# Kernel tuning notes

Measured on AMD Instinct MI355X. Metric: run time of the kernel, lower is better.

## Reference

```python
import jax, jax.numpy as jnp
import numpy as np

VX, VY, VZ = 0.2, 0.2, 4.0
PCR = (0.0, -40.0, -3.0, 70.4, 40.0, 1.0)
X_OFF = VX / 2 + PCR[0]
Y_OFF = VY / 2 + PCR[1]
Z_OFF = VZ / 2 + PCR[2]
BN_EPS = 1e-3
N_POINTS = 600000
N_VOXELS = 60000
CANVAS_X, CANVAS_Y = 352, 400  # (70.4-0)/0.2, (40-(-40))/0.2


def setup_inputs() -> dict:
    key = jax.random.key(0)
    ks = jax.random.split(key, 8)
    rng = np.random.default_rng(0)
    # pick N_VOXELS distinct occupied voxels on the BEV canvas
    lin = rng.permutation(CANVAS_X * CANVAS_Y)[:N_VOXELS]
    inv = rng.integers(0, N_VOXELS, size=N_POINTS)
    inv[:N_VOXELS] = np.arange(N_VOXELS)  # guarantee every voxel occupied
    pv = lin[inv]
    coors = np.zeros((N_POINTS, 4), np.int32)  # (batch, z, y, x)
    coors[:, 3] = pv % CANVAS_X
    coors[:, 2] = pv // CANVAS_X
    # point features: xyz inside point cloud range + intensity
    px = jax.random.uniform(ks[0], (N_POINTS,), minval=PCR[0], maxval=PCR[3])
    py = jax.random.uniform(ks[1], (N_POINTS,), minval=PCR[1], maxval=PCR[4])
    pz = jax.random.uniform(ks[2], (N_POINTS,), minval=PCR[2], maxval=PCR[5])
    pi = jax.random.uniform(ks[3], (N_POINTS,))
    features = jnp.stack([px, py, pz, pi], axis=1)
    return {
        'features': features,
        'w0': jax.random.normal(ks[4], (10, 64)) * 0.3,
        'g0': jnp.ones((64,)),
        'b0': jnp.zeros((64,)),
        'w1': jax.random.normal(ks[5], (128, 128)) * 0.08,
        'g1': jnp.ones((128,)),
        'b1': jnp.zeros((128,)),
        'coors': jnp.asarray(coors),
        'unq_inv': jnp.asarray(inv.astype(np.int32)),
        'num_voxels': N_VOXELS,
    }


def _bn_relu(x, g, b):
    # BN1d training-mode forward: biased batch stats, eps=1e-3
    mu = jnp.mean(x, axis=0)
    var = jnp.mean(jnp.square(x - mu), axis=0)
    return jax.nn.relu((x - mu) * jax.lax.rsqrt(var + BN_EPS) * g + b)


def reference(features, w0, g0, b0, w1, g1, b1, coors, unq_inv, num_voxels):
    n = features.shape[0]
    cf = coors.astype(features.dtype)
    # cluster center: scatter-mean of point features per voxel, gathered back
    vsum = jax.ops.segment_sum(features, unq_inv, num_segments=num_voxels)
    cnt = jax.ops.segment_sum(jnp.ones((n, 1), features.dtype), unq_inv,
                              num_segments=num_voxels)
    voxel_mean = vsum / jnp.maximum(cnt, 1.0)
    f_cluster = features[:, :3] - voxel_mean[unq_inv][:, :3]
    # offset to voxel center (coors layout: batch, z, y, x)
    f_center = jnp.stack([
        features[:, 0] - (cf[:, 3] * VX + X_OFF),
        features[:, 1] - (cf[:, 2] * VY + Y_OFF),
        features[:, 2] - (cf[:, 1] * VZ + Z_OFF),
    ], axis=1)
    x = jnp.concatenate([features, f_cluster, f_center], axis=1)  # [N,10]
    # VFE layer 0 + scatter-max pool + gather-concat
    p0 = _bn_relu(x @ w0, g0, b0)                                  # [N,64]
    v0 = jax.ops.segment_max(p0, unq_inv, num_segments=num_voxels)
    x1 = jnp.concatenate([p0, v0[unq_inv]], axis=1)                # [N,128]
    # VFE layer 1 + final scatter-max pool
    p1 = _bn_relu(x1 @ w1, g1, b1)                                 # [N,128]
    voxel_feats = jax.ops.segment_max(p1, unq_inv, num_segments=num_voxels)
    return voxel_feats  # [M,128]
```

## Files before the change

kernel.cpp:

```cpp
#include <hip/hip_runtime.h>
#include <hip/hip_bf16.h>


typedef __attribute__((ext_vector_type(8))) short bf16x8;
typedef __attribute__((ext_vector_type(4))) float f32x4;
typedef __attribute__((ext_vector_type(4))) int i32x4;
typedef unsigned short u16;
typedef unsigned int u32;

#define RSP 72
#define SCB 2048
#define SPW0 6
#define SPW1 6

__device__ __forceinline__ float bf2f(u16 u) { return __uint_as_float(((u32)u) << 16); }
__device__ __forceinline__ u16 f2bfbits(float f) {
  __hip_bfloat16 h = __float2bfloat16(f);
  return __builtin_bit_cast(u16, h);
}
__device__ __forceinline__ float ldf(const void* p, int i, int flag) {
  return flag ? bf2f(((const u16*)p)[i]) : ((const float*)p)[i];
}
__device__ __forceinline__ u32 encf(float f) {
  u32 b = __float_as_uint(f);
  return b ^ ((u32)(((int)b) >> 31) | 0x80000000u);
}
__device__ __forceinline__ float decf(u32 k) {
  u32 b = (k & 0x80000000u) ? (k ^ 0x80000000u) : ~k;
  return __uint_as_float(b);
}
__device__ __forceinline__ u32 bflyu(u32 x) {
  x = max(x, (u32)__shfl_xor((int)x, 16));
  x = max(x, (u32)__shfl_xor((int)x, 32));
  return x;
}
__device__ __forceinline__ float bflyf(float x) {
  x = fmaxf(x, __shfl_xor(x, 16));
  x = fmaxf(x, __shfl_xor(x, 32));
  return x;
}
__device__ __forceinline__ bf16x8 pack8(float4 a, float4 b) {
  bf16x8 r;
  r[0] = (short)f2bfbits(a.x); r[1] = (short)f2bfbits(a.y);
  r[2] = (short)f2bfbits(a.z); r[3] = (short)f2bfbits(a.w);
  r[4] = (short)f2bfbits(b.x); r[5] = (short)f2bfbits(b.y);
  r[6] = (short)f2bfbits(b.z); r[7] = (short)f2bfbits(b.w);
  return r;
}

__global__ void k_probe(const u32* __restrict__ g0bits, int* __restrict__ flag) {
  if (threadIdx.x == 0 && blockIdx.x == 0)
    flag[0] = (g0bits[0] == 0x3F800000u) ? 0 : 1;
}

__global__ __launch_bounds__(256) void k_pre(
    const void* __restrict__ w0p, const void* __restrict__ w1p,
    const void* __restrict__ g1p,
    u16* __restrict__ w0t, u16* __restrict__ w1t, u32* __restrict__ gsign,
    float4* __restrict__ z4a, long nza4,
    float4* __restrict__ keysws, float4* __restrict__ doutp, long nzk4,
    const int* __restrict__ flagp) {
  const int t = threadIdx.x;
  const int flag = flagp[0];
  if (blockIdx.x == 0) {
    for (int i = t; i < 2048; i += 256) {
      int c = i >> 5, k = i & 31;
      w0t[i] = (k < 10) ? f2bfbits(ldf(w0p, k * 64 + c, flag)) : (u16)0;
    }
    for (int i = t; i < 16384; i += 256) {
      int c = i >> 7, k = i & 127;
      w1t[i] = f2bfbits(ldf(w1p, k * 128 + c, flag));
    }
    if (t < 128) gsign[t] = (ldf(g1p, t, flag) < 0.f) ? 0xFFFFFFFFu : 0u;
  } else {
    float4* keys4 = flag ? keysws : doutp;
    const long total = nza4 + nzk4;
    const long nth = (long)(gridDim.x - 1) * 256;
    const float4 z = {0.f, 0.f, 0.f, 0.f};
    for (long i = (long)(blockIdx.x - 1) * 256 + t; i < total; i += nth) {
      if (i < nza4) z4a[i] = z; else keys4[i - nza4] = z;
    }
  }
}

__global__ __launch_bounds__(256) void k_hist(const int* __restrict__ inv,
                                              unsigned* __restrict__ vcnt, int n) {
  const int stride = gridDim.x * blockDim.x;
  for (int p = blockIdx.x * blockDim.x + threadIdx.x; p < n; p += stride)
    atomicAdd(&vcnt[inv[p]], 1u);
}

__global__ __launch_bounds__(256) void k_scanA(const unsigned* __restrict__ vcnt,
                                               unsigned* __restrict__ bsum, int M) {
  __shared__ unsigned sh[4];
  const int t = threadIdx.x;
  long base = (long)blockIdx.x * SCB;
  unsigned s = 0;
  for (int i = t; i < SCB; i += 256) {
    long idx = base + i;
    s += (idx < M) ? vcnt[idx] : 0u;
  }
  #pragma unroll
  for (int off = 1; off < 64; off <<= 1) s += __shfl_xor(s, off);
  if ((t & 63) == 0) sh[t >> 6] = s;
  __syncthreads();
  if (t == 0) bsum[blockIdx.x] = sh[0] + sh[1] + sh[2] + sh[3];
}

__global__ __launch_bounds__(256) void k_scanB(const unsigned* __restrict__ bsum,
                                               unsigned* __restrict__ boff, int nb) {
  __shared__ unsigned sh[256];
  const int t = threadIdx.x;
  unsigned loc[8];
  unsigned s = 0;
  #pragma unroll
  for (int j = 0; j < 8; ++j) {
    int i = t * 8 + j;
    loc[j] = (i < nb) ? bsum[i] : 0u;
    s += loc[j];
  }
  sh[t] = s; __syncthreads();
  for (int off = 1; off < 256; off <<= 1) {
    unsigned add = (t >= off) ? sh[t - off] : 0u;
    __syncthreads();
    sh[t] += add;
    __syncthreads();
  }
  unsigned excl = sh[t] - s;
  #pragma unroll
  for (int j = 0; j < 8; ++j) {
    int i = t * 8 + j;
    if (i < nb) { boff[i] = excl; excl += loc[j]; }
  }
}

__global__ __launch_bounds__(256) void k_scanC(const unsigned* __restrict__ vcnt,
                                               const unsigned* __restrict__ boff,
                                               unsigned* __restrict__ voff, int M) {
  __shared__ unsigned sh[256];
  const int t = threadIdx.x;
  long base = (long)blockIdx.x * SCB;
  unsigned loc[8];
  unsigned s = 0;
  #pragma unroll
  for (int j = 0; j < 8; ++j) {
    long i = base + t * 8 + j;
    loc[j] = (i < M) ? vcnt[i] : 0u;
    s += loc[j];
  }
  sh[t] = s; __syncthreads();
  for (int off = 1; off < 256; off <<= 1) {
    unsigned add = (t >= off) ? sh[t - off] : 0u;
    __syncthreads();
    sh[t] += add;
    __syncthreads();
  }
  unsigned excl = sh[t] - s + boff[blockIdx.x];
  #pragma unroll
  for (int j = 0; j < 8; ++j) {
    long i = base + t * 8 + j;
    if (i < M) { voff[i] = excl; excl += loc[j]; }
  }
}

__global__ __launch_bounds__(256) void k_fill2(
    const void* __restrict__ feat, const int4* __restrict__ coors4,
    const int* __restrict__ inv, const unsigned* __restrict__ voff,
    unsigned* __restrict__ wcur, u32* __restrict__ rec,
    const int* __restrict__ flagp, int n) {
  const int flag = flagp[0];
  const int stride = gridDim.x * blockDim.x;
  for (int p = blockIdx.x * blockDim.x + threadIdx.x; p < n; p += stride) {
    float fx, fy, fz, fi;
    if (flag) {
      ushort4 f = ((const ushort4*)feat)[p];
      fx = bf2f(f.x); fy = bf2f(f.y); fz = bf2f(f.z); fi = bf2f(f.w);
    } else {
      float4 f = ((const float4*)feat)[p];
      fx = f.x; fy = f.y; fz = f.z; fi = f.w;
    }
    int4 c = coors4[p];
    u32 cp = ((u32)(c.y & 0xFFF) << 20) | ((u32)(c.z & 0x3FF) << 10) | (u32)(c.w & 0x3FF);
    int v = inv[p];
    unsigned pos = voff[v] + atomicAdd(&wcur[v], 1u);
    uint4* dst = (uint4*)(rec + (long)pos * 8);
    uint4 q0 = {__float_as_uint(fx), __float_as_uint(fy), __float_as_uint(fz), __float_as_uint(fi)};
    uint4 q1 = {cp, (u32)v, 0u, 0u};
    dst[0] = q0;
    dst[1] = q1;
  }
}

__global__ __launch_bounds__(256) void k_vsum2(
    const u32* __restrict__ rec, const unsigned* __restrict__ voff,
    const unsigned* __restrict__ vcnt, float* __restrict__ vsum, int M) {
  const int v = blockIdx.x * 256 + threadIdx.x;
  if (v >= M) return;
  const unsigned o = voff[v], c = vcnt[v];
  float sx = 0.f, sy = 0.f, sz = 0.f;
  for (unsigned j = 0; j < c; ++j) {
    const float* rp = (const float*)(rec + (long)(o + j) * 8);
    sx += rp[0]; sy += rp[1]; sz += rp[2];
  }
  vsum[3 * v + 0] = sx;
  vsum[3 * v + 1] = sy;
  vsum[3 * v + 2] = sz;
}

__global__ __launch_bounds__(256) void k_fillx2(
    const u32* __restrict__ rec, const float* __restrict__ vsum,
    const unsigned* __restrict__ vcnt,
    u32* __restrict__ xpk, float* __restrict__ stat0acc, int n) {
  float acc[65];
  #pragma unroll
  for (int j = 0; j < 65; ++j) acc[j] = 0.f;
  const int t = threadIdx.x;
  const int stride = gridDim.x * blockDim.x;
  for (int pos = blockIdx.x * blockDim.x + t; pos < n; pos += stride) {
    const u32* rp = rec + (long)pos * 8;
    uint4 q0 = *(const uint4*)rp;
    uint4 q1 = *(const uint4*)(rp + 4);
    float px = __uint_as_float(q0.x), py = __uint_as_float(q0.y);
    float pz = __uint_as_float(q0.z), pi = __uint_as_float(q0.w);
    const u32 cp = q1.x;
    const int v = (int)q1.y;
    unsigned cn = vcnt[v];
    float ic = 1.f / (float)(cn ? cn : 1u);
    float mx = vsum[3 * v + 0] * ic, my = vsum[3 * v + 1] * ic, mz = vsum[3 * v + 2] * ic;
    float x[10];
    x[0] = px; x[1] = py; x[2] = pz; x[3] = pi;
    x[4] = px - mx; x[5] = py - my; x[6] = pz - mz;
    x[7] = px - ((float)(cp & 0x3FFu) * 0.2f + 0.1f);
    x[8] = py - ((float)((cp >> 10) & 0x3FFu) * 0.2f - 39.9f);
    x[9] = pz - ((float)((cp >> 20) & 0xFFFu) * 4.0f - 1.0f);
    int k = 0;
    #pragma unroll
    for (int a = 0; a < 10; ++a) acc[k++] += x[a];
    #pragma unroll
    for (int a = 0; a < 10; ++a) {
      #pragma unroll
      for (int b = a; b < 10; ++b) acc[k++] += x[a] * x[b];
    }
    u32 u[5];
    #pragma unroll
    for (int j = 0; j < 5; ++j)
      u[j] = (u32)f2bfbits(x[2 * j]) | ((u32)f2bfbits(x[2 * j + 1]) << 16);
    uint4* dst = (uint4*)(xpk + (long)pos * 8);
    uint4 o0 = {u[0], u[1], u[2], u[3]};
    uint4 o1 = {u[4], (u32)v, 0u, 0u};
    dst[0] = o0;
    dst[1] = o1;
  }
  __shared__ float red[65];
  if (t < 65) red[t] = 0.f;
  __syncthreads();
  const int lane = t & 63;
  #pragma unroll
  for (int j = 0; j < 65; ++j) {
    float s = acc[j];
    #pragma unroll
    for (int off = 1; off < 64; off <<= 1) s += __shfl_xor(s, off);
    if (lane == 0) atomicAdd(&red[j], s);
  }
  __syncthreads();
  if (t < 65) atomicAdd(&stat0acc[t], red[t]);
}

__global__ void k_bn0fin(const float* __restrict__ stat0acc,
                         const void* __restrict__ w0p,
                         const void* __restrict__ g0p,
                         const void* __restrict__ b0p,
                         float* __restrict__ a0, float* __restrict__ c0,
                         const int* __restrict__ flagp, int n) {
  const int flag = flagp[0];
  __shared__ float tot[65];
  const int t = threadIdx.x;
  if (t < 65) tot[t] = stat0acc[t];
  __syncthreads();
  if (t < 64) {
    const float invN = 1.0f / (float)n;
    float w[10];
    #pragma unroll
    for (int i = 0; i < 10; ++i) w[i] = ldf(w0p, i * 64 + t, flag);
    float mu = 0.f;
    #pragma unroll
    for (int i = 0; i < 10; ++i) mu += tot[i] * w[i];
    mu *= invN;
    float e2 = 0.f;
    int k = 10;
    #pragma unroll
    for (int a = 0; a < 10; ++a) {
      #pragma unroll
      for (int b = a; b < 10; ++b) {
        float term = tot[k++] * invN * w[a] * w[b];
        e2 += (a == b) ? term : 2.0f * term;
      }
    }
    float var = fmaxf(e2 - mu * mu, 0.f);
    float rs = 1.0f / sqrtf(var + 1e-3f);
    float aa = ldf(g0p, t, flag) * rs;
    a0[t] = aa;
    c0[t] = ldf(b0p, t, flag) - mu * aa;
  }
}

__device__ __forceinline__ bf16x8 l0frag(const u32* __restrict__ xpk,
                                         long grow, long n, int kg) {
  i32x4 ai = {0, 0, 0, 0};
  if (grow < n) {
    const u32* rp = xpk + grow * 8;
    if (kg == 0) {
      uint4 q = *(const uint4*)rp;
      ai[0] = (int)q.x; ai[1] = (int)q.y; ai[2] = (int)q.z; ai[3] = (int)q.w;
    } else if (kg == 1) {
      ai[0] = (int)rp[4];
    }
  }
  return __builtin_bit_cast(bf16x8, ai);
}

__global__ __launch_bounds__(256) void k_l0vox(
    const u32* __restrict__ xpk, const u16* __restrict__ w0t,
    const float* __restrict__ a0, const float* __restrict__ c0,
    float* __restrict__ v0, long n, long nseg, int M) {
  __shared__ int vxs[64];
  __shared__ float pval[2][64];
  __shared__ int pvox[2];
  const int t = threadIdx.x, lane = t & 63, w = t >> 6;
  const int cl = lane & 15, kg = lane >> 4;
  const bf16x8 bw = *(const bf16x8*)(w0t + (16 * w + cl) * 32 + 8 * kg);
  const float al = a0[16 * w + cl], be = c0[16 * w + cl];
  const f32x4 fz = {0.f, 0.f, 0.f, 0.f};
  int curv = -2; float cm = 0.f;
  bool first = true; int fvox = -2; float fcm = 0.f;
  int lastid = -2;
  const long segbase = (long)blockIdx.x * SPW0;
  for (int s = 0; s < SPW0; ++s) {
    const long seg = segbase + s;
    if (seg >= nseg) break;
    const long jb = seg * 64;
    if (t < 64) vxs[t] = (jb + t < n) ? (int)xpk[(jb + t) * 8 + 5] : M;
    __syncthreads();
    for (int mt = 0; mt < 4; ++mt) {
      const long grow = jb + 16 * mt + cl;
      bf16x8 av = l0frag(xpk, grow, n, kg);
      f32x4 a = __builtin_amdgcn_mfma_f32_16x16x32_bf16(av, bw, fz, 0, 0, 0);
      float y[4];
      #pragma unroll
      for (int i2 = 0; i2 < 4; ++i2)
        y[i2] = fmaxf(fmaf(a[i2], al, be), 0.f);
      const int rb = 16 * mt;
      const int rid = vxs[rb + cl];
      const int prid = (cl == 0) ? lastid : vxs[rb + cl - 1];
      const u32 starts = (u32)(__ballot(rid != prid) & 0xFFFFull) | 0x10000u;
      int r = 0;
      while (r < 16) {
        const u32 above = starts & (0xFFFFFFFFu << (r + 1));
        const int e = __ffs(above) - 2;
        const int vrun = __shfl(rid, r);
        float pm = 0.f;
        #pragma unroll
        for (int i2 = 0; i2 < 4; ++i2) {
          const int row = 4 * kg + i2;
          pm = (row >= r && row <= e) ? fmaxf(pm, y[i2]) : pm;
        }
        pm = bflyf(pm);
        if (vrun == curv) cm = fmaxf(cm, pm);
        else {
          if (curv >= 0 && curv < M) {
            if (first) { fvox = curv; fcm = cm; first = false; }
            else if (kg == 0) v0[(long)curv * 64 + 16 * w + cl] = cm;
          }
          curv = vrun; cm = pm;
        }
        r = e + 1;
      }
      lastid = vxs[rb + 15];
    }
    __syncthreads();
  }
  if (t == 0) { pvox[0] = fvox; pvox[1] = curv; }
  if (kg == 0) { pval[0][16 * w + cl] = fcm; pval[1][16 * w + cl] = cm; }
  __syncthreads();
  if (t < 64) {
    int vox = -2; float val = 0.f; bool afirst = true;
    for (int e2 = 0; e2 < 2; ++e2) {
      int ev = pvox[e2];
      if (ev < 0 || ev >= M) continue;
      float evv = pval[e2][t];
      if (ev == vox) val = fmaxf(val, evv);
      else {
        if (vox >= 0) {
          if (afirst) { atomicMax((int*)&v0[(long)vox * 64 + t], __float_as_int(val)); afirst = false; }
          else v0[(long)vox * 64 + t] = val;
        }
        vox = ev; val = evv;
      }
    }
    if (vox >= 0) atomicMax((int*)&v0[(long)vox * 64 + t], __float_as_int(val));
  }
}

__global__ __launch_bounds__(256) void k_v0cvt(const float4* __restrict__ v0,
                                               bf16x8* __restrict__ v0b, long n8) {
  const long stride = (long)gridDim.x * blockDim.x;
  for (long i = (long)blockIdx.x * blockDim.x + threadIdx.x; i < n8; i += stride) {
    float4 f0 = v0[2 * i];
    float4 f1 = v0[2 * i + 1];
    v0b[i] = pack8(f0, f1);
  }
}

__global__ __launch_bounds__(256) void k_vfe1vox(
    const u32* __restrict__ xpk, const u16* __restrict__ w0t,
    const float* __restrict__ a0, const float* __restrict__ c0,
    const u16* __restrict__ w1t, const u32* __restrict__ gsign,
    const u16* __restrict__ v0b,
    u32* __restrict__ keysws, u32* __restrict__ doutk,
    float* __restrict__ stat1acc,
    const int* __restrict__ flagp, long n, long nseg, int M) {
  const int flag = flagp[0];
  u32* keys = flag ? keysws : doutk;
  __shared__ u16 stg[64 * RSP];
  __shared__ int vxs[64];
  __shared__ u32 pval[2][128];
  __shared__ int pvox[2];
  const int t = threadIdx.x, lane = t & 63, w = t >> 6;
  const int cl = lane & 15, kg = lane >> 4;
  const int ct0 = 2 * w, ct1 = 2 * w + 1;
  bf16x8 bw[4];
  float al[4], be[4];
  #pragma unroll
  for (int ct = 0; ct < 4; ++ct) {
    bw[ct] = *(const bf16x8*)(w0t + (16 * ct + cl) * 32 + 8 * kg);
    al[ct] = a0[16 * ct + cl];
    be[ct] = c0[16 * ct + cl];
  }
  const u32 gs0 = gsign[16 * ct0 + cl], gs1 = gsign[16 * ct1 + cl];
  const u16* wr0 = w1t + (16 * ct0 + cl) * 128 + 8 * kg;
  const u16* wr1 = w1t + (16 * ct1 + cl) * 128 + 8 * kg;
  float ssum0 = 0.f, ssq0 = 0.f, ssum1 = 0.f, ssq1 = 0.f;
  const f32x4 fz = {0.f, 0.f, 0.f, 0.f};
  int curv = -2; u32 cm0 = 0, cm1 = 0;
  bool first = true; int fvox = -2; u32 fm0 = 0, fm1 = 0;
  int lastid = -2;
  const long segbase = (long)blockIdx.x * SPW1;

  for (int s = 0; s < SPW1; ++s) {
    const long seg = segbase + s;
    if (seg >= nseg) break;
    const long jb = seg * 64;
    if (t < 64) vxs[t] = (jb + t < n) ? (int)xpk[(jb + t) * 8 + 5] : M;
    {
      const long grow = jb + 16 * w + cl;
      bf16x8 av = l0frag(xpk, grow, n, kg);
      #pragma unroll
      for (int ct = 0; ct < 4; ++ct) {
        f32x4 a = __builtin_amdgcn_mfma_f32_16x16x32_bf16(av, bw[ct], fz, 0, 0, 0);
        #pragma unroll
        for (int i2 = 0; i2 < 4; ++i2) {
          const int lr = 16 * w + 4 * kg + i2;
          float y = fmaxf(fmaf(a[i2], al[ct], be[ct]), 0.f);
          if (jb + lr >= n) y = 0.f;
          stg[lr * RSP + 16 * ct + cl] = f2bfbits(y);
        }
      }
    }
    __syncthreads();
    for (int q = 0; q < 4; ++q) {
      const int lr = 16 * q + cl;
      bf16x8 afr0 = *(const bf16x8*)&stg[lr * RSP + 8 * kg];
      bf16x8 afr1 = *(const bf16x8*)&stg[lr * RSP + 32 + 8 * kg];
      const int vv = vxs[lr];
      const u16* vb = v0b + (long)vv * 64;
      bf16x8 afr2 = *(const bf16x8*)(vb + 8 * kg);
      bf16x8 afr3 = *(const bf16x8*)(vb + 32 + 8 * kg);
      f32x4 acc0 = fz, acc1 = fz;
      {
        bf16x8 b0 = *(const bf16x8*)(wr0);
        bf16x8 b1 = *(const bf16x8*)(wr0 + 32);
        bf16x8 b2 = *(const bf16x8*)(wr0 + 64);
        bf16x8 b3 = *(const bf16x8*)(wr0 + 96);
        acc0 = __builtin_amdgcn_mfma_f32_16x16x32_bf16(afr0, b0, acc0, 0, 0, 0);
        acc0 = __builtin_amdgcn_mfma_f32_16x16x32_bf16(afr1, b1, acc0, 0, 0, 0);
        acc0 = __builtin_amdgcn_mfma_f32_16x16x32_bf16(afr2, b2, acc0, 0, 0, 0);
        acc0 = __builtin_amdgcn_mfma_f32_16x16x32_bf16(afr3, b3, acc0, 0, 0, 0);
      }
      {
        bf16x8 b0 = *(const bf16x8*)(wr1);
        bf16x8 b1 = *(const bf16x8*)(wr1 + 32);
        bf16x8 b2 = *(const bf16x8*)(wr1 + 64);
        bf16x8 b3 = *(const bf16x8*)(wr1 + 96);
        acc1 = __builtin_amdgcn_mfma_f32_16x16x32_bf16(afr0, b0, acc1, 0, 0, 0);
        acc1 = __builtin_amdgcn_mfma_f32_16x16x32_bf16(afr1, b1, acc1, 0, 0, 0);
        acc1 = __builtin_amdgcn_mfma_f32_16x16x32_bf16(afr2, b2, acc1, 0, 0, 0);
        acc1 = __builtin_amdgcn_mfma_f32_16x16x32_bf16(afr3, b3, acc1, 0, 0, 0);
      }
      u32 e0[4], e1[4];
      #pragma unroll
      for (int i2 = 0; i2 < 4; ++i2) {
        float ya = acc0[i2], yb = acc1[i2];
        if (jb + 16 * q + 4 * kg + i2 >= n) { ya = 0.f; yb = 0.f; }
        ssum0 += ya; ssq0 += ya * ya;
        ssum1 += yb; ssq1 += yb * yb;
        e0[i2] = encf(ya) ^ gs0;
        e1[i2] = encf(yb) ^ gs1;
      }
      const int rb = 16 * q;
      const int rid = vxs[rb + cl];
      const int prid = (cl == 0) ? lastid : vxs[rb + cl - 1];
      const u32 starts = (u32)(__ballot(rid != prid) & 0xFFFFull) | 0x10000u;
      int r = 0;
      while (r < 16) {
        const u32 above = starts & (0xFFFFFFFFu << (r + 1));
        const int e = __ffs(above) - 2;
        const int vrun = __shfl(rid, r);
        u32 p0m = 0, p1m = 0;
        #pragma unroll
        for (int i2 = 0; i2 < 4; ++i2) {
          const int row = 4 * kg + i2;
          const bool in = (row >= r) && (row <= e);
          p0m = in ? max(p0m, e0[i2]) : p0m;
          p1m = in ? max(p1m, e1[i2]) : p1m;
        }
        p0m = bflyu(p0m);
        p1m = bflyu(p1m);
        if (vrun == curv) { cm0 = max(cm0, p0m); cm1 = max(cm1, p1m); }
        else {
          if (curv >= 0 && curv < M) {
            if (first) { fvox = curv; fm0 = cm0; fm1 = cm1; first = false; }
            else if (kg == 0) {
              u32* row = keys + (long)curv * 128;
              row[16 * ct0 + cl] = cm0;
              row[16 * ct1 + cl] = cm1;
            }
          }
          curv = vrun; cm0 = p0m; cm1 = p1m;
        }
        r = e + 1;
      }
      lastid = vxs[rb + 15];
    }
    __syncthreads();
  }
  if (t == 0) { pvox[0] = fvox; pvox[1] = curv; }
  if (kg == 0) {
    pval[0][16 * ct0 + cl] = fm0; pval[0][16 * ct1 + cl] = fm1;
    pval[1][16 * ct0 + cl] = cm0; pval[1][16 * ct1 + cl] = cm1;
  }
  __syncthreads();
  if (t < 128) {
    int vox = -2; u32 val = 0; bool afirst = true;
    for (int e2 = 0; e2 < 2; ++e2) {
      int ev = pvox[e2];
      if (ev < 0 || ev >= M) continue;
      u32 evv = pval[e2][t];
      if (ev == vox) val = max(val, evv);
      else {
        if (vox >= 0) {
          if (afirst) { atomicMax(&keys[(long)vox * 128 + t], val); afirst = false; }
          else keys[(long)vox * 128 + t] = val;
        }
        vox = ev; val = evv;
      }
    }
    if (vox >= 0) atomicMax(&keys[(long)vox * 128 + t], val);
  }
  ssum0 += __shfl_xor(ssum0, 16); ssum0 += __shfl_xor(ssum0, 32);
  ssq0 += __shfl_xor(ssq0, 16); ssq0 += __shfl_xor(ssq0, 32);
  ssum1 += __shfl_xor(ssum1, 16); ssum1 += __shfl_xor(ssum1, 32);
  ssq1 += __shfl_xor(ssq1, 16); ssq1 += __shfl_xor(ssq1, 32);
  if (kg == 0) {
    atomicAdd(&stat1acc[16 * ct0 + cl], ssum0);
    atomicAdd(&stat1acc[16 * ct1 + cl], ssum1);
    atomicAdd(&stat1acc[128 + 16 * ct0 + cl], ssq0);
    atomicAdd(&stat1acc[128 + 16 * ct1 + cl], ssq1);
  }
}

__global__ void k_bn1fin(const float* __restrict__ stat1acc,
                         const void* __restrict__ g1p,
                         const void* __restrict__ b1p,
                         float* __restrict__ a1, float* __restrict__ c1,
                         const int* __restrict__ flagp, int n) {
  const int flag = flagp[0];
  const int c = threadIdx.x;
  float s = stat1acc[c];
  float q = stat1acc[128 + c];
  const float invN = 1.0f / (float)n;
  float mu = s * invN;
  float var = fmaxf(q * invN - mu * mu, 0.f);
  float rs = 1.0f / sqrtf(var + 1e-3f);
  float aa = ldf(g1p, c, flag) * rs;
  a1[c] = aa;
  c1[c] = ldf(b1p, c, flag) - mu * aa;
}

__global__ __launch_bounds__(256) void k_fin(
    const u32* __restrict__ keysws, u32* __restrict__ doutk,
    const float* __restrict__ a1, const float* __restrict__ c1,
    const u32* __restrict__ gsign, void* __restrict__ dout,
    const int* __restrict__ flagp, int m32) {
  const int flag = flagp[0];
  const uint4* src = (const uint4*)(flag ? keysws : doutk);
  const int stride = gridDim.x * blockDim.x;
  for (int i = blockIdx.x * blockDim.x + threadIdx.x; i < m32; i += stride) {
    uint4 k = src[i];
    const int cb = (i * 4) & 127;
    float z0 = fmaxf(fmaf(decf(k.x ^ gsign[cb + 0]), a1[cb + 0], c1[cb + 0]), 0.f);
    float z1 = fmaxf(fmaf(decf(k.y ^ gsign[cb + 1]), a1[cb + 1], c1[cb + 1]), 0.f);
    float z2 = fmaxf(fmaf(decf(k.z ^ gsign[cb + 2]), a1[cb + 2], c1[cb + 2]), 0.f);
    float z3 = fmaxf(fmaf(decf(k.w ^ gsign[cb + 3]), a1[cb + 3], c1[cb + 3]), 0.f);
    if (flag) {
      ushort4 o;
      o.x = f2bfbits(z0); o.y = f2bfbits(z1); o.z = f2bfbits(z2); o.w = f2bfbits(z3);
      ((ushort4*)dout)[i] = o;
    } else {
      float4 o = {z0, z1, z2, z3};
      ((float4*)dout)[i] = o;
    }
  }
}

extern "C" void kernel_launch(void* const* d_in, const int* in_sizes, int n_in,
                              void* d_out, int out_size, void* d_ws, size_t ws_size,
                              hipStream_t stream) {
  (void)n_in; (void)ws_size;
  const int n = in_sizes[0] / 4;
  const int M = out_size / 128;
  const long nseg = (n + 63) >> 6;
  const int nb = (M + SCB - 1) / SCB;
  const int nblk0 = (int)((nseg + SPW0 - 1) / SPW0);
  const int nblk1 = (int)((nseg + SPW1 - 1) / SPW1);
  const int nbv = (M + 255) / 256;
  if (n <= 0 || M <= 0) return;

  const void* feat = d_in[0];
  const void* w0p = d_in[1];
  const void* g0p = d_in[2];
  const void* b0p = d_in[3];
  const void* w1p = d_in[4];
  const void* g1p = d_in[5];
  const void* b1p = d_in[6];
  const int4* coors4 = (const int4*)d_in[7];
  const int* inv = (const int*)d_in[8];

  char* wsb = (char*)d_ws;
  long off = 0;
  auto alloc = [&](long bytes) -> void* {
    void* p = wsb + off;
    off = (off + bytes + 255) & ~255L;
    return p;
  };
  int* flagp = (int*)alloc(256);
  float* a0 = (float*)alloc(256);
  float* c0 = (float*)alloc(256);
  float* a1 = (float*)alloc(512);
  float* c1 = (float*)alloc(512);
  u32* gsign = (u32*)alloc(512);
  u16* w0t = (u16*)alloc(2048 * 2);
  u16* w1t = (u16*)alloc(16384 * 2);
  unsigned* bsum = (unsigned*)alloc(2048 * 4);
  unsigned* boff = (unsigned*)alloc(2048 * 4);
  unsigned* voff = (unsigned*)alloc((long)M * 4);
  float* vsum = (float*)alloc((long)M * 3 * 4);
  u32* rec = (u32*)alloc((long)nseg * 64 * 32);
  u32* xpk = (u32*)alloc((long)nseg * 64 * 32);
  u16* v0b = (u16*)alloc((long)(M + 1) * 64 * 2);
  const long nza = 384L + M + (long)(M + 1) * 64 + M;
  float* zbase = (float*)alloc(((nza + 3) / 4) * 16);
  float* stat0acc = zbase;
  float* stat1acc = zbase + 80;
  unsigned* vcnt = (unsigned*)(zbase + 384);
  float* v0 = (float*)(vcnt + M);
  unsigned* wcur = (unsigned*)(v0 + (long)(M + 1) * 64);
  u32* keysws = (u32*)alloc((long)M * 128 * 4);

  hipLaunchKernelGGL(k_probe, dim3(1), dim3(64), 0, stream, (const u32*)g0p, flagp);
  hipLaunchKernelGGL(k_pre, dim3(2048), dim3(256), 0, stream,
                     w0p, w1p, g1p, w0t, w1t, gsign,
                     (float4*)zbase, (nza + 3) / 4,
                     (float4*)keysws, (float4*)d_out, (long)M * 32, flagp);
  hipLaunchKernelGGL(k_hist, dim3(1024), dim3(256), 0, stream, inv, vcnt, n);
  hipLaunchKernelGGL(k_scanA, dim3(nb), dim3(256), 0, stream, vcnt, bsum, M);
  hipLaunchKernelGGL(k_scanB, dim3(1), dim3(256), 0, stream, bsum, boff, nb);
  hipLaunchKernelGGL(k_scanC, dim3(nb), dim3(256), 0, stream, vcnt, boff, voff, M);
  hipLaunchKernelGGL(k_fill2, dim3(1024), dim3(256), 0, stream,
                     feat, coors4, inv, voff, wcur, rec, flagp, n);
  hipLaunchKernelGGL(k_vsum2, dim3(nbv), dim3(256), 0, stream,
                     rec, voff, vcnt, vsum, M);
  hipLaunchKernelGGL(k_fillx2, dim3(1024), dim3(256), 0, stream,
                     rec, vsum, vcnt, xpk, stat0acc, n);
  hipLaunchKernelGGL(k_bn0fin, dim3(1), dim3(128), 0, stream,
                     stat0acc, w0p, g0p, b0p, a0, c0, flagp, n);
  hipLaunchKernelGGL(k_l0vox, dim3(nblk0), dim3(256), 0, stream,
                     xpk, w0t, a0, c0, v0, (long)n, nseg, M);
  hipLaunchKernelGGL(k_v0cvt, dim3(512), dim3(256), 0, stream,
                     (const float4*)v0, (bf16x8*)v0b, (long)(M + 1) * 8);
  hipLaunchKernelGGL(k_vfe1vox, dim3(nblk1), dim3(256), 0, stream,
                     xpk, w0t, a0, c0, w1t, gsign, v0b,
                     keysws, (u32*)d_out, stat1acc, flagp, (long)n, nseg, M);
  hipLaunchKernelGGL(k_bn1fin, dim3(1), dim3(128), 0, stream,
                     stat1acc, g1p, b1p, a1, c1, flagp, n);
  hipLaunchKernelGGL(k_fin, dim3(1024), dim3(256), 0, stream,
                     keysws, (u32*)d_out, a1, c1, gsign, d_out, flagp, M * 32);
}
```

Baseline: 383.2 us.

## Give each wavefront its own segments in layer-0 and layer-1 voxel kernels

Restructures k_l0vox and k_vfe1vox so each wavefront handles its own run of 64-point segments and computes all output channels itself. Previously the four waves of a block split channels and shared staging through LDS with block-wide barriers. Segment voxel ids are now read per lane and neighbours found with shuffles, and layer-1 stages its activation through a per-wave LDS tile with the MFMA operands swapped. The goal is to remove __syncthreads and cross-wave LDS traffic, at the cost of more registers per thread and twice as many boundary atomicMax operations per block.

```diff
diff --git a/kernel.cpp b/kernel.cpp
--- a/kernel.cpp
+++ b/kernel.cpp
@@ -8,10 +8,10 @@
 typedef unsigned short u16;
 typedef unsigned int u32;
 
-#define RSP 72
 #define SCB 2048
 #define SPW0 6
 #define SPW1 6
+#define TRS 72
 
 __device__ __forceinline__ float bf2f(u16 u) { return __uint_as_float(((u32)u) << 16); }
 __device__ __forceinline__ u16 f2bfbits(float f) {
@@ -39,13 +39,8 @@
   x = fmaxf(x, __shfl_xor(x, 32));
   return x;
 }
-__device__ __forceinline__ bf16x8 pack8(float4 a, float4 b) {
-  bf16x8 r;
-  r[0] = (short)f2bfbits(a.x); r[1] = (short)f2bfbits(a.y);
-  r[2] = (short)f2bfbits(a.z); r[3] = (short)f2bfbits(a.w);
-  r[4] = (short)f2bfbits(b.x); r[5] = (short)f2bfbits(b.y);
-  r[6] = (short)f2bfbits(b.z); r[7] = (short)f2bfbits(b.w);
-  return r;
+__device__ __forceinline__ u32 packbf(float a, float b) {
+  return (u32)f2bfbits(a) | ((u32)f2bfbits(b) << 16);
 }
 
 __global__ void k_probe(const u32* __restrict__ g0bits, int* __restrict__ flag) {
@@ -244,7 +239,7 @@
     u32 u[5];
     #pragma unroll
     for (int j = 0; j < 5; ++j)
-      u[j] = (u32)f2bfbits(x[2 * j]) | ((u32)f2bfbits(x[2 * j + 1]) << 16);
+      u[j] = packbf(x[2 * j], x[2 * j + 1]);
     uint4* dst = (uint4*)(xpk + (long)pos * 8);
     uint4 o0 = {u[0], u[1], u[2], u[3]};
     uint4 o1 = {u[4], (u32)v, 0u, 0u};
@@ -323,91 +318,109 @@
     const u32* __restrict__ xpk, const u16* __restrict__ w0t,
     const float* __restrict__ a0, const float* __restrict__ c0,
     float* __restrict__ v0, long n, long nseg, int M) {
-  __shared__ int vxs[64];
-  __shared__ float pval[2][64];
-  __shared__ int pvox[2];
   const int t = threadIdx.x, lane = t & 63, w = t >> 6;
   const int cl = lane & 15, kg = lane >> 4;
-  const bf16x8 bw = *(const bf16x8*)(w0t + (16 * w + cl) * 32 + 8 * kg);
-  const float al = a0[16 * w + cl], be = c0[16 * w + cl];
+  bf16x8 bw[4];
+  float al[4], be[4];
+  #pragma unroll
+  for (int ct = 0; ct < 4; ++ct) {
+    bw[ct] = *(const bf16x8*)(w0t + (16 * ct + cl) * 32 + 8 * kg);
+    al[ct] = a0[16 * ct + cl];
+    be[ct] = c0[16 * ct + cl];
+  }
   const f32x4 fz = {0.f, 0.f, 0.f, 0.f};
-  int curv = -2; float cm = 0.f;
-  bool first = true; int fvox = -2; float fcm = 0.f;
+  int curv = -2;
+  float cm[4] = {0.f, 0.f, 0.f, 0.f};
+  bool first = true; int fvox = -2;
+  float fm[4] = {0.f, 0.f, 0.f, 0.f};
   int lastid = -2;
-  const long segbase = (long)blockIdx.x * SPW0;
+  const long seg0 = ((long)blockIdx.x * 4 + w) * SPW0;
   for (int s = 0; s < SPW0; ++s) {
-    const long seg = segbase + s;
+    const long seg = seg0 + s;
     if (seg >= nseg) break;
     const long jb = seg * 64;
-    if (t < 64) vxs[t] = (jb + t < n) ? (int)xpk[(jb + t) * 8 + 5] : M;
-    __syncthreads();
+    #pragma unroll
     for (int mt = 0; mt < 4; ++mt) {
-      const long grow = jb + 16 * mt + cl;
-      bf16x8 av = l0frag(xpk, grow, n, kg);
-      f32x4 a = __builtin_amdgcn_mfma_f32_16x16x32_bf16(av, bw, fz, 0, 0, 0);
-      float y[4];
+      const long prow = jb + 16 * mt + cl;
+      const int rid = (prow < n) ? (int)xpk[prow * 8 + 5] : M;
+      bf16x8 av = l0frag(xpk, prow, n, kg);
+      float y[4][4];
       #pragma unroll
-      for (int i2 = 0; i2 < 4; ++i2)
-        y[i2] = fmaxf(fmaf(a[i2], al, be), 0.f);
-      const int rb = 16 * mt;
-      const int rid = vxs[rb + cl];
-      const int prid = (cl == 0) ? lastid : vxs[rb + cl - 1];
+      for (int ct = 0; ct < 4; ++ct) {
+        f32x4 p = __builtin_amdgcn_mfma_f32_16x16x32_bf16(av, bw[ct], fz, 0, 0, 0);
+        #pragma unroll
+        for (int i2 = 0; i2 < 4; ++i2) {
+          float yy = fmaxf(fmaf(p[i2], al[ct], be[ct]), 0.f);
+          if (jb + 16 * mt + 4 * kg + i2 >= n) yy = 0.f;
+          y[ct][i2] = yy;
+        }
+      }
+      int prid = __shfl(rid, lane - 1);
+      if (cl == 0) prid = lastid;
       const u32 starts = (u32)(__ballot(rid != prid) & 0xFFFFull) | 0x10000u;
       int r = 0;
       while (r < 16) {
         const u32 above = starts & (0xFFFFFFFFu << (r + 1));
         const int e = __ffs(above) - 2;
         const int vrun = __shfl(rid, r);
-        float pm = 0.f;
+        float pm[4];
         #pragma unroll
-        for (int i2 = 0; i2 < 4; ++i2) {
-          const int row = 4 * kg + i2;
-          pm = (row >= r && row <= e) ? fmaxf(pm, y[i2]) : pm;
+        for (int ct = 0; ct < 4; ++ct) {
+          float q = 0.f;
+          #pragma unroll
+          for (int i2 = 0; i2 < 4; ++i2) {
+            const int row = 4 * kg + i2;
+            q = (row >= r && row <= e) ? fmaxf(q, y[ct][i2]) : q;
+          }
+          pm[ct] = bflyf(q);
         }
-        pm = bflyf(pm);
-        if (vrun == curv) cm = fmaxf(cm, pm);
-        else {
+        if (vrun == curv) {
+          #pragma unroll
+          for (int ct = 0; ct < 4; ++ct) cm[ct] = fmaxf(cm[ct], pm[ct]);
+        } else {
           if (curv >= 0 && curv < M) {
-            if (first) { fvox = curv; fcm = cm; first = false; }
-            else if (kg == 0) v0[(long)curv * 64 + 16 * w + cl] = cm;
+            if (first) {
+              fvox = curv;
+              #pragma unroll
+              for (int ct = 0; ct < 4; ++ct) fm[ct] = cm[ct];
+              first = false;
+            } else if (kg == 0) {
+              #pragma unroll
+              for (int ct = 0; ct < 4; ++ct)
+                v0[(long)curv * 64 + 16 * ct + cl] = cm[ct];
+            }
           }
-          curv = vrun; cm = pm;
+          curv = vrun;
+          #pragma unroll
+          for (int ct = 0; ct < 4; ++ct) cm[ct] = pm[ct];
         }
         r = e + 1;
       }
-      lastid = vxs[rb + 15];
-    }
-    __syncthreads();
-  }
-  if (t == 0) { pvox[0] = fvox; pvox[1] = curv; }
-  if (kg == 0) { pval[0][16 * w + cl] = fcm; pval[1][16 * w + cl] = cm; }
-  __syncthreads();
-  if (t < 64) {
-    int vox = -2; float val = 0.f; bool afirst = true;
-    for (int e2 = 0; e2 < 2; ++e2) {
-      int ev = pvox[e2];
-      if (ev < 0 || ev >= M) continue;
-      float evv = pval[e2][t];
-      if (ev == vox) val = fmaxf(val, evv);
-      else {
-        if (vox >= 0) {
-          if (afirst) { atomicMax((int*)&v0[(long)vox * 64 + t], __float_as_int(val)); afirst = false; }
-          else v0[(long)vox * 64 + t] = val;
-        }
-        vox = ev; val = evv;
-      }
-    }
-    if (vox >= 0) atomicMax((int*)&v0[(long)vox * 64 + t], __float_as_int(val));
-  }
-}
-
-__global__ __launch_bounds__(256) void k_v0cvt(const float4* __restrict__ v0,
-                                               bf16x8* __restrict__ v0b, long n8) {
+      lastid = __shfl(rid, 15);
+    }
+  }
+  if (fvox >= 0 && fvox < M && kg == 0) {
+    #pragma unroll
+    for (int ct = 0; ct < 4; ++ct)
+      atomicMax((int*)&v0[(long)fvox * 64 + 16 * ct + cl], __float_as_int(fm[ct]));
+  }
+  if (curv >= 0 && curv < M && kg == 0) {
+    #pragma unroll
+    for (int ct = 0; ct < 4; ++ct)
+      atomicMax((int*)&v0[(long)curv * 64 + 16 * ct + cl], __float_as_int(cm[ct]));
+  }
+}
+
+__global__ __launch_bounds__(256) void k_v0cvt(const float* __restrict__ v0,
+                                               u32* __restrict__ v0b32, long n8) {
   const long stride = (long)gridDim.x * blockDim.x;
   for (long i = (long)blockIdx.x * blockDim.x + threadIdx.x; i < n8; i += stride) {
-    float4 f0 = v0[2 * i];
-    float4 f1 = v0[2 * i + 1];
-    v0b[i] = pack8(f0, f1);
+    float4 f0 = *(const float4*)(v0 + 8 * i);
+    float4 f1 = *(const float4*)(v0 + 8 * i + 4);
+    uint4 o;
+    o.x = packbf(f0.x, f0.y); o.y = packbf(f0.z, f0.w);
+    o.z = packbf(f1.x, f1.y); o.w = packbf(f1.z, f1.w);
+    *(uint4*)(v0b32 + 4 * i) = o;
   }
 }
 
@@ -421,160 +434,209 @@
     const int* __restrict__ flagp, long n, long nseg, int M) {
   const int flag = flagp[0];
   u32* keys = flag ? keysws : doutk;
-  __shared__ u16 stg[64 * RSP];
-  __shared__ int vxs[64];
-  __shared__ u32 pval[2][128];
-  __shared__ int pvox[2];
+  __shared__ __align__(16) u16 tbuf[4][16 * TRS];
   const int t = threadIdx.x, lane = t & 63, w = t >> 6;
   const int cl = lane & 15, kg = lane >> 4;
-  const int ct0 = 2 * w, ct1 = 2 * w + 1;
+  u16* tb = tbuf[w];
   bf16x8 bw[4];
-  float al[4], be[4];
+  f32x4 alq[4], beq[4];
   #pragma unroll
   for (int ct = 0; ct < 4; ++ct) {
     bw[ct] = *(const bf16x8*)(w0t + (16 * ct + cl) * 32 + 8 * kg);
-    al[ct] = a0[16 * ct + cl];
-    be[ct] = c0[16 * ct + cl];
-  }
-  const u32 gs0 = gsign[16 * ct0 + cl], gs1 = gsign[16 * ct1 + cl];
-  const u16* wr0 = w1t + (16 * ct0 + cl) * 128 + 8 * kg;
-  const u16* wr1 = w1t + (16 * ct1 + cl) * 128 + 8 * kg;
-  float ssum0 = 0.f, ssq0 = 0.f, ssum1 = 0.f, ssq1 = 0.f;
+    alq[ct] = *(const f32x4*)(a0 + 16 * ct + 4 * kg);
+    beq[ct] = *(const f32x4*)(c0 + 16 * ct + 4 * kg);
+  }
+  u32 gsv[8];
+  #pragma unroll
+  for (int ct = 0; ct < 8; ++ct) gsv[ct] = gsign[16 * ct + cl];
+  float ssum[8], ssq[8];
+  #pragma unroll
+  for (int j = 0; j < 8; ++j) { ssum[j] = 0.f; ssq[j] = 0.f; }
   const f32x4 fz = {0.f, 0.f, 0.f, 0.f};
-  int curv = -2; u32 cm0 = 0, cm1 = 0;
-  bool first = true; int fvox = -2; u32 fm0 = 0, fm1 = 0;
+
+  int curvA = -2, curvB = -2;
+  u32 cmA[4] = {0, 0, 0, 0}, cmB[4] = {0, 0, 0, 0};
+  bool firstA = true, firstB = true;
+  int fvoxA = -2, fvoxB = -2;
+  u32 fmA[4] = {0, 0, 0, 0}, fmB[4] = {0, 0, 0, 0};
   int lastid = -2;
-  const long segbase = (long)blockIdx.x * SPW1;
+  const long seg0 = ((long)blockIdx.x * 4 + w) * SPW1;
 
   for (int s = 0; s < SPW1; ++s) {
-    const long seg = segbase + s;
+    const long seg = seg0 + s;
     if (seg >= nseg) break;
     const long jb = seg * 64;
-    if (t < 64) vxs[t] = (jb + t < n) ? (int)xpk[(jb + t) * 8 + 5] : M;
-    {
-      const long grow = jb + 16 * w + cl;
-      bf16x8 av = l0frag(xpk, grow, n, kg);
+    #pragma unroll
+    for (int mt = 0; mt < 4; ++mt) {
+      const long prow = jb + 16 * mt + cl;
+      const int rid = (prow < n) ? (int)xpk[prow * 8 + 5] : M;
+      bf16x8 av = l0frag(xpk, prow, n, kg);
       #pragma unroll
       for (int ct = 0; ct < 4; ++ct) {
-        f32x4 a = __builtin_amdgcn_mfma_f32_16x16x32_bf16(av, bw[ct], fz, 0, 0, 0);
+        f32x4 p = __builtin_amdgcn_mfma_f32_16x16x32_bf16(bw[ct], av, fz, 0, 0, 0);
+        float y0 = fmaxf(fmaf(p[0], alq[ct][0], beq[ct][0]), 0.f);
+        float y1 = fmaxf(fmaf(p[1], alq[ct][1], beq[ct][1]), 0.f);
+        float y2 = fmaxf(fmaf(p[2], alq[ct][2], beq[ct][2]), 0.f);
+        float y3 = fmaxf(fmaf(p[3], alq[ct][3], beq[ct][3]), 0.f);
+        if (prow >= n) { y0 = 0.f; y1 = 0.f; y2 = 0.f; y3 = 0.f; }
+        uint2 pr = {packbf(y0, y1), packbf(y2, y3)};
+        *(uint2*)&tb[cl * TRS + 16 * ct + 4 * kg] = pr;
+      }
+      bf16x8 afr0 = *(const bf16x8*)&tb[cl * TRS + 8 * kg];
+      bf16x8 afr1 = *(const bf16x8*)&tb[cl * TRS + 32 + 8 * kg];
+      const u16* vb = v0b + (long)rid * 64;
+      bf16x8 afr2 = *(const bf16x8*)(vb + 8 * kg);
+      bf16x8 afr3 = *(const bf16x8*)(vb + 32 + 8 * kg);
+      bool padr[4];
+      #pragma unroll
+      for (int i2 = 0; i2 < 4; ++i2) padr[i2] = (jb + 16 * mt + 4 * kg + i2 >= n);
+      int prid = __shfl(rid, lane - 1);
+      if (cl == 0) prid = lastid;
+      const u32 starts = (u32)(__ballot(rid != prid) & 0xFFFFull) | 0x10000u;
+      {
+        u32 eh[4][4];
         #pragma unroll
-        for (int i2 = 0; i2 < 4; ++i2) {
-          const int lr = 16 * w + 4 * kg + i2;
-          float y = fmaxf(fmaf(a[i2], al[ct], be[ct]), 0.f);
-          if (jb + lr >= n) y = 0.f;
-          stg[lr * RSP + 16 * ct + cl] = f2bfbits(y);
+        for (int ct = 0; ct < 4; ++ct) {
+          const u16* wr = w1t + (16 * ct + cl) * 128 + 8 * kg;
+          f32x4 a = fz;
+          a = __builtin_amdgcn_mfma_f32_16x16x32_bf16(afr0, *(const bf16x8*)(wr), a, 0, 0, 0);
+          a = __builtin_amdgcn_mfma_f32_16x16x32_bf16(afr1, *(const bf16x8*)(wr + 32), a, 0, 0, 0);
+          a = __builtin_amdgcn_mfma_f32_16x16x32_bf16(afr2, *(const bf16x8*)(wr + 64), a, 0, 0, 0);
+          a = __builtin_amdgcn_mfma_f32_16x16x32_bf16(afr3, *(const bf16x8*)(wr + 96), a, 0, 0, 0);
+          #pragma unroll
+          for (int i2 = 0; i2 < 4; ++i2) {
+            float yy = padr[i2] ? 0.f : a[i2];
+            ssum[ct] += yy; ssq[ct] += yy * yy;
+            eh[ct][i2] = encf(yy) ^ gsv[ct];
+          }
+        }
+        int r = 0;
+        while (r < 16) {
+          const u32 above = starts & (0xFFFFFFFFu << (r + 1));
+          const int e = __ffs(above) - 2;
+          const int vrun = __shfl(rid, r);
+          u32 pm[4];
+          #pragma unroll
+          for (int ct = 0; ct < 4; ++ct) {
+            u32 q = 0;
+            #pragma unroll
+            for (int i2 = 0; i2 < 4; ++i2) {
+              const int row = 4 * kg + i2;
+              q = (row >= r && row <= e) ? max(q, eh[ct][i2]) : q;
+            }
+            pm[ct] = bflyu(q);
+          }
+          if (vrun == curvA) {
+            #pragma unroll
+            for (int ct = 0; ct < 4; ++ct) cmA[ct] = max(cmA[ct], pm[ct]);
+          } else {
+            if (curvA >= 0 && curvA < M) {
+              if (firstA) {
+                fvoxA = curvA;
+                #pragma unroll
+                for (int ct = 0; ct < 4; ++ct) fmA[ct] = cmA[ct];
+                firstA = false;
+              } else if (kg == 0) {
+                u32* row = keys + (long)curvA * 128;
+                #pragma unroll
+                for (int ct = 0; ct < 4; ++ct) row[16 * ct + cl] = cmA[ct];
+              }
+            }
+            curvA = vrun;
+            #pragma unroll
+            for (int ct = 0; ct < 4; ++ct) cmA[ct] = pm[ct];
+          }
+          r = e + 1;
         }
       }
-    }
-    __syncthreads();
-    for (int q = 0; q < 4; ++q) {
-      const int lr = 16 * q + cl;
-      bf16x8 afr0 = *(const bf16x8*)&stg[lr * RSP + 8 * kg];
-      bf16x8 afr1 = *(const bf16x8*)&stg[lr * RSP + 32 + 8 * kg];
-      const int vv = vxs[lr];
-      const u16* vb = v0b + (long)vv * 64;
-      bf16x8 afr2 = *(const bf16x8*)(vb + 8 * kg);
-      bf16x8 afr3 = *(const bf16x8*)(vb + 32 + 8 * kg);
-      f32x4 acc0 = fz, acc1 = fz;
       {
-        bf16x8 b0 = *(const bf16x8*)(wr0);
-        bf16x8 b1 = *(const bf16x8*)(wr0 + 32);
-        bf16x8 b2 = *(const bf16x8*)(wr0 + 64);
-        bf16x8 b3 = *(const bf16x8*)(wr0 + 96);
-        acc0 = __builtin_amdgcn_mfma_f32_16x16x32_bf16(afr0, b0, acc0, 0, 0, 0);
-        acc0 = __builtin_amdgcn_mfma_f32_16x16x32_bf16(afr1, b1, acc0, 0, 0, 0);
-        acc0 = __builtin_amdgcn_mfma_f32_16x16x32_bf16(afr2, b2, acc0, 0, 0, 0);
-        acc0 = __builtin_amdgcn_mfma_f32_16x16x32_bf16(afr3, b3, acc0, 0, 0, 0);
+        u32 eh[4][4];
+        #pragma unroll
+        for (int ct = 0; ct < 4; ++ct) {
+          const u16* wr = w1t + (16 * (ct + 4) + cl) * 128 + 8 * kg;
+          f32x4 a = fz;
+          a = __builtin_amdgcn_mfma_f32_16x16x32_bf16(afr0, *(const bf16x8*)(wr), a, 0, 0, 0);
+          a = __builtin_amdgcn_mfma_f32_16x16x32_bf16(afr1, *(const bf16x8*)(wr + 32), a, 0, 0, 0);
+          a = __builtin_amdgcn_mfma_f32_16x16x32_bf16(afr2, *(const bf16x8*)(wr + 64), a, 0, 0, 0);
+          a = __builtin_amdgcn_mfma_f32_16x16x32_bf16(afr3, *(const bf16x8*)(wr + 96), a, 0, 0, 0);
+          #pragma unroll
+          for (int i2 = 0; i2 < 4; ++i2) {
+            float yy = padr[i2] ? 0.f : a[i2];
+            ssum[ct + 4] += yy; ssq[ct + 4] += yy * yy;
+            eh[ct][i2] = encf(yy) ^ gsv[ct + 4];
+          }
+        }
+        int r = 0;
+        while (r < 16) {
+          const u32 above = starts & (0xFFFFFFFFu << (r + 1));
+          const int e = __ffs(above) - 2;
+          const int vrun = __shfl(rid, r);
+          u32 pm[4];
+          #pragma unroll
+          for (int ct = 0; ct < 4; ++ct) {
+            u32 q = 0;
+            #pragma unroll
+            for (int i2 = 0; i2 < 4; ++i2) {
+              const int row = 4 * kg + i2;
+              q = (row >= r && row <= e) ? max(q, eh[ct][i2]) : q;
+            }
+            pm[ct] = bflyu(q);
+          }
+          if (vrun == curvB) {
+            #pragma unroll
+            for (int ct = 0; ct < 4; ++ct) cmB[ct] = max(cmB[ct], pm[ct]);
+          } else {
+            if (curvB >= 0 && curvB < M) {
+              if (firstB) {
+                fvoxB = curvB;
+                #pragma unroll
+                for (int ct = 0; ct < 4; ++ct) fmB[ct] = cmB[ct];
+                firstB = false;
+              } else if (kg == 0) {
+                u32* row = keys + (long)curvB * 128;
+                #pragma unroll
+                for (int ct = 0; ct < 4; ++ct) row[64 + 16 * ct + cl] = cmB[ct];
+              }
+            }
+            curvB = vrun;
+            #pragma unroll
+            for (int ct = 0; ct < 4; ++ct) cmB[ct] = pm[ct];
+          }
+          r = e + 1;
+        }
       }
-      {
-        bf16x8 b0 = *(const bf16x8*)(wr1);
-        bf16x8 b1 = *(const bf16x8*)(wr1 + 32);
-        bf16x8 b2 = *(const bf16x8*)(wr1 + 64);
-        bf16x8 b3 = *(const bf16x8*)(wr1 + 96);
-        acc1 = __builtin_amdgcn_mfma_f32_16x16x32_bf16(afr0, b0, acc1, 0, 0, 0);
-        acc1 = __builtin_amdgcn_mfma_f32_16x16x32_bf16(afr1, b1, acc1, 0, 0, 0);
-        acc1 = __builtin_amdgcn_mfma_f32_16x16x32_bf16(afr2, b2, acc1, 0, 0, 0);
-        acc1 = __builtin_amdgcn_mfma_f32_16x16x32_bf16(afr3, b3, acc1, 0, 0, 0);
-      }
-      u32 e0[4], e1[4];
-      #pragma unroll
-      for (int i2 = 0; i2 < 4; ++i2) {
-        float ya = acc0[i2], yb = acc1[i2];
-        if (jb + 16 * q + 4 * kg + i2 >= n) { ya = 0.f; yb = 0.f; }
-        ssum0 += ya; ssq0 += ya * ya;
-        ssum1 += yb; ssq1 += yb * yb;
-        e0[i2] = encf(ya) ^ gs0;
-        e1[i2] = encf(yb) ^ gs1;
-      }
-      const int rb = 16 * q;
-      const int rid = vxs[rb + cl];
-      const int prid = (cl == 0) ? lastid : vxs[rb + cl - 1];
-      const u32 starts = (u32)(__ballot(rid != prid) & 0xFFFFull) | 0x10000u;
-      int r = 0;
-      while (r < 16) {
-        const u32 above = starts & (0xFFFFFFFFu << (r + 1));
-        const int e = __ffs(above) - 2;
-        const int vrun = __shfl(rid, r);
-        u32 p0m = 0, p1m = 0;
-        #pragma unroll
-        for (int i2 = 0; i2 < 4; ++i2) {
-          const int row = 4 * kg + i2;
-          const bool in = (row >= r) && (row <= e);
-          p0m = in ? max(p0m, e0[i2]) : p0m;
-          p1m = in ? max(p1m, e1[i2]) : p1m;
-        }
-        p0m = bflyu(p0m);
-        p1m = bflyu(p1m);
-        if (vrun == curv) { cm0 = max(cm0, p0m); cm1 = max(cm1, p1m); }
-        else {
-          if (curv >= 0 && curv < M) {
-            if (first) { fvox = curv; fm0 = cm0; fm1 = cm1; first = false; }
-            else if (kg == 0) {
-              u32* row = keys + (long)curv * 128;
-              row[16 * ct0 + cl] = cm0;
-              row[16 * ct1 + cl] = cm1;
-            }
-          }
-          curv = vrun; cm0 = p0m; cm1 = p1m;
-        }
-        r = e + 1;
-      }
-      lastid = vxs[rb + 15];
-    }
-    __syncthreads();
-  }
-  if (t == 0) { pvox[0] = fvox; pvox[1] = curv; }
-  if (kg == 0) {
-    pval[0][16 * ct0 + cl] = fm0; pval[0][16 * ct1 + cl] = fm1;
-    pval[1][16 * ct0 + cl] = cm0; pval[1][16 * ct1 + cl] = cm1;
-  }
-  __syncthreads();
-  if (t < 128) {
-    int vox = -2; u32 val = 0; bool afirst = true;
-    for (int e2 = 0; e2 < 2; ++e2) {
-      int ev = pvox[e2];
-      if (ev < 0 || ev >= M) continue;
-      u32 evv = pval[e2][t];
-      if (ev == vox) val = max(val, evv);
-      else {
-        if (vox >= 0) {
-          if (afirst) { atomicMax(&keys[(long)vox * 128 + t], val); afirst = false; }
-          else keys[(long)vox * 128 + t] = val;
-        }
-        vox = ev; val = evv;
-      }
-    }
-    if (vox >= 0) atomicMax(&keys[(long)vox * 128 + t], val);
-  }
-  ssum0 += __shfl_xor(ssum0, 16); ssum0 += __shfl_xor(ssum0, 32);
-  ssq0 += __shfl_xor(ssq0, 16); ssq0 += __shfl_xor(ssq0, 32);
-  ssum1 += __shfl_xor(ssum1, 16); ssum1 += __shfl_xor(ssum1, 32);
-  ssq1 += __shfl_xor(ssq1, 16); ssq1 += __shfl_xor(ssq1, 32);
-  if (kg == 0) {
-    atomicAdd(&stat1acc[16 * ct0 + cl], ssum0);
-    atomicAdd(&stat1acc[16 * ct1 + cl], ssum1);
-    atomicAdd(&stat1acc[128 + 16 * ct0 + cl], ssq0);
-    atomicAdd(&stat1acc[128 + 16 * ct1 + cl], ssq1);
+      lastid = __shfl(rid, 15);
+    }
+  }
+  if (fvoxA >= 0 && fvoxA < M && kg == 0) {
+    u32* row = keys + (long)fvoxA * 128;
+    #pragma unroll
+    for (int ct = 0; ct < 4; ++ct) atomicMax(&row[16 * ct + cl], fmA[ct]);
+  }
+  if (curvA >= 0 && curvA < M && kg == 0) {
+    u32* row = keys + (long)curvA * 128;
+    #pragma unroll
+    for (int ct = 0; ct < 4; ++ct) atomicMax(&row[16 * ct + cl], cmA[ct]);
+  }
+  if (fvoxB >= 0 && fvoxB < M && kg == 0) {
+    u32* row = keys + (long)fvoxB * 128;
+    #pragma unroll
+    for (int ct = 0; ct < 4; ++ct) atomicMax(&row[64 + 16 * ct + cl], fmB[ct]);
+  }
+  if (curvB >= 0 && curvB < M && kg == 0) {
+    u32* row = keys + (long)curvB * 128;
+    #pragma unroll
+    for (int ct = 0; ct < 4; ++ct) atomicMax(&row[64 + 16 * ct + cl], cmB[ct]);
+  }
+  #pragma unroll
+  for (int ct = 0; ct < 8; ++ct) {
+    float sa = ssum[ct], qa = ssq[ct];
+    sa += __shfl_xor(sa, 16); sa += __shfl_xor(sa, 32);
+    qa += __shfl_xor(qa, 16); qa += __shfl_xor(qa, 32);
+    if (kg == 0) {
+      atomicAdd(&stat1acc[16 * ct + cl], sa);
+      atomicAdd(&stat1acc[128 + 16 * ct + cl], qa);
+    }
   }
 }
 
@@ -630,8 +692,8 @@
   const int M = out_size / 128;
   const long nseg = (n + 63) >> 6;
   const int nb = (M + SCB - 1) / SCB;
-  const int nblk0 = (int)((nseg + SPW0 - 1) / SPW0);
-  const int nblk1 = (int)((nseg + SPW1 - 1) / SPW1);
+  const int nblk0 = (int)((nseg + 4 * SPW0 - 1) / (4 * SPW0));
+  const int nblk1 = (int)((nseg + 4 * SPW1 - 1) / (4 * SPW1));
   const int nbv = (M + 255) / 256;
   if (n <= 0 || M <= 0) return;
 
@@ -696,7 +758,7 @@
   hipLaunchKernelGGL(k_l0vox, dim3(nblk0), dim3(256), 0, stream,
                      xpk, w0t, a0, c0, v0, (long)n, nseg, M);
   hipLaunchKernelGGL(k_v0cvt, dim3(512), dim3(256), 0, stream,
-                     (const float4*)v0, (bf16x8*)v0b, (long)(M + 1) * 8);
+                     v0, (u32*)v0b, (long)(M + 1) * 8);
   hipLaunchKernelGGL(k_vfe1vox, dim3(nblk1), dim3(256), 0, stream,
                      xpk, w0t, a0, c0, w1t, gsign, v0b,
                      keysws, (u32*)d_out, stat1acc, flagp, (long)n, nseg, M);
```

New measurement: 580.8 us. +51.6%, slower.
